# Kernel tuning notes

Measured on AMD Instinct MI355X. Metric: run time of the kernel, lower is better.

## Reference

```python
import jax, jax.numpy as jnp
import numpy as np
from jax import lax

B = 32768
IMG = 28
K = 3
OUT_HW = IMG - K + 1  # 26
FLAT = OUT_HW * OUT_HW  # 676
HID = 300
NCLS = 10


def setup_inputs() -> dict:
    key = jax.random.key(0)
    ks = jax.random.split(key, 8)
    x = jax.random.normal(ks[0], (B, IMG * IMG), dtype=jnp.float32)
    conv_w = jax.random.normal(ks[1], (K, K), dtype=jnp.float32) * 0.1
    # Linear params stored as (in, out) so forward is h @ W + b
    W1 = jax.random.normal(ks[2], (FLAT, HID), dtype=jnp.float32) * 0.04
    b1 = jnp.zeros((HID,), dtype=jnp.float32)
    W2 = jax.random.normal(ks[3], (HID, HID), dtype=jnp.float32) * 0.06
    b2 = jnp.zeros((HID,), dtype=jnp.float32)
    W3 = jax.random.normal(ks[4], (HID, NCLS), dtype=jnp.float32) * 0.06
    b3 = jnp.zeros((NCLS,), dtype=jnp.float32)
    return {"x": x, "conv_w": conv_w, "W1": W1, "b1": b1,
            "W2": W2, "b2": b2, "W3": W3, "b3": b3}


def reference(x, conv_w, W1, b1, W2, b2, W3, b3):
    b = x.shape[0]
    img = x.reshape(b, 1, IMG, IMG)  # NCHW
    # Valid cross-correlation with 3x3 kernel -> [B,1,26,26]
    y = lax.conv_general_dilated(
        img, conv_w[None, None, :, :], window_strides=(1, 1), padding="VALID",
        dimension_numbers=("NCHW", "OIHW", "NCHW"))
    h = y.reshape(b, FLAT)
    h = jax.nn.relu(h @ W1 + b1)
    h = jax.nn.relu(h @ W2 + b2)
    return h @ W3 + b3
```

## Files before the change

### kernel.cpp

```cpp
#include <hip/hip_runtime.h>


typedef __bf16 bf16_t;
typedef __bf16 bf16x8 __attribute__((ext_vector_type(8)));
typedef float  f32x4  __attribute__((ext_vector_type(4)));

#define MFMA16(a, b, c) __builtin_amdgcn_mfma_f32_16x16x32_bf16((a), (b), (c), 0, 0, 0)

#define W1F_ELEMS (25 * 20 * 64 * 8)
#define W2F_ELEMS (10 * 20 * 64 * 8)
#define W3F_ELEMS (10 * 1 * 64 * 8)

__global__ void prep_weights(const float* __restrict__ conv_w,
                             const float* __restrict__ W1,
                             const float* __restrict__ W2,
                             const float* __restrict__ W3,
                             bf16_t* __restrict__ W1f,
                             bf16_t* __restrict__ W2f,
                             bf16_t* __restrict__ W3f) {
    int idx = blockIdx.x * 256 + threadIdx.x;
    if (idx < 800 * 320) {
        int k = idx / 320;
        int n = idx - k * 320;
        float v = 0.0f;
        if (k < 784 && n < 300) {
            int py = k / 28;
            int px = k - py * 28;
#pragma unroll
            for (int ky = 0; ky < 3; ++ky) {
                int oy = py - ky;
                if (oy < 0 || oy > 25) continue;
#pragma unroll
                for (int kx = 0; kx < 3; ++kx) {
                    int ox = px - kx;
                    if (ox < 0 || ox > 25) continue;
                    v += conv_w[ky * 3 + kx] * W1[(oy * 26 + ox) * 300 + n];
                }
            }
        }
        int kc = k >> 5, quad = (k >> 3) & 3, j = k & 7;
        int nt = n >> 4, nin = n & 15;
        W1f[(((kc * 20 + nt) * 64 + quad * 16 + nin) << 3) + j] = (bf16_t)v;
    } else if (idx < 800 * 320 + 320 * 320) {
        int i2 = idx - 800 * 320;
        int k = i2 / 320;
        int n = i2 - k * 320;
        float v = (k < 300 && n < 300) ? W2[k * 300 + n] : 0.0f;
        int kc = k >> 5, quad = (k >> 3) & 3, j = k & 7;
        int nt = n >> 4, nin = n & 15;
        W2f[(((kc * 20 + nt) * 64 + quad * 16 + nin) << 3) + j] = (bf16_t)v;
    } else if (idx < 800 * 320 + 320 * 320 + 320 * 16) {
        int i3 = idx - (800 * 320 + 320 * 320);
        int k = i3 / 16;
        int n = i3 - k * 16;
        float v = (k < 300 && n < 10) ? W3[k * 10 + n] : 0.0f;
        int kc = k >> 5, quad = (k >> 3) & 3, j = k & 7;
        W3f[(((kc * 64) + quad * 16 + n) << 3) + j] = (bf16_t)v;
    }
}

__global__ __launch_bounds__(256, 2) void fused_mlp(
    const float* __restrict__ x, const float* __restrict__ b1,
    const float* __restrict__ b2, const float* __restrict__ b3,
    const bf16x8* __restrict__ W1f, const bf16x8* __restrict__ W2f,
    const bf16x8* __restrict__ W3f, float* __restrict__ out) {
    __shared__ bf16x8 bufA[4 * 64];
    __shared__ bf16x8 hbuf[10 * 4 * 64];

    const int tid = threadIdx.x;
    const int w = tid >> 6;
    const int l = tid & 63;
    const int r0 = blockIdx.x * 64;

    const int sr = tid >> 2;
    const int sg = tid & 3;
    const int s_mt = sr >> 4;
    const int s_lane = sg * 16 + (sr & 15);
    const float* xrow = x + (size_t)(r0 + sr) * 784;

    f32x4 acc[4][5];
#pragma unroll
    for (int mt = 0; mt < 4; ++mt)
#pragma unroll
        for (int nt = 0; nt < 5; ++nt) acc[mt][nt] = (f32x4){0.f, 0.f, 0.f, 0.f};

    float4 u0, u1;
    {
        int k0 = sg * 8;
        const float4* p = (const float4*)(xrow + k0);
        u0 = p[0];
        u1 = p[1];
    }
    for (int kc = 0; kc < 25; ++kc) {
        bf16x8 af;
        af[0] = (bf16_t)u0.x; af[1] = (bf16_t)u0.y;
        af[2] = (bf16_t)u0.z; af[3] = (bf16_t)u0.w;
        af[4] = (bf16_t)u1.x; af[5] = (bf16_t)u1.y;
        af[6] = (bf16_t)u1.z; af[7] = (bf16_t)u1.w;
        bufA[s_mt * 64 + s_lane] = af;
        __syncthreads();
        if (kc + 1 < 25) {
            int k0 = (kc + 1) * 32 + sg * 8;
            if (k0 < 784) {
                const float4* p = (const float4*)(xrow + k0);
                u0 = p[0];
                u1 = p[1];
            } else {
                u0 = make_float4(0.f, 0.f, 0.f, 0.f);
                u1 = make_float4(0.f, 0.f, 0.f, 0.f);
            }
        }
        bf16x8 a0 = bufA[0 * 64 + l];
        bf16x8 a1 = bufA[1 * 64 + l];
        bf16x8 a2 = bufA[2 * 64 + l];
        bf16x8 a3 = bufA[3 * 64 + l];
        const bf16x8* wb = W1f + (size_t)(kc * 20 + w * 5) * 64 + l;
#pragma unroll
        for (int nt = 0; nt < 5; ++nt) {
            bf16x8 b = wb[nt * 64];
            acc[0][nt] = MFMA16(a0, b, acc[0][nt]);
            acc[1][nt] = MFMA16(a1, b, acc[1][nt]);
            acc[2][nt] = MFMA16(a2, b, acc[2][nt]);
            acc[3][nt] = MFMA16(a3, b, acc[3][nt]);
        }
        __syncthreads();
    }

    {
        bf16_t* hb = (bf16_t*)hbuf;
#pragma unroll
        for (int nt = 0; nt < 5; ++nt) {
            int n = (w * 5 + nt) * 16 + (l & 15);
            float bias = (n < 300) ? b1[n] : 0.0f;
            int kc2 = n >> 5, quad = (n >> 3) & 3, j = n & 7;
#pragma unroll
            for (int mt = 0; mt < 4; ++mt) {
#pragma unroll
                for (int r = 0; r < 4; ++r) {
                    int row15 = (l >> 4) * 4 + r;
                    float v = acc[mt][nt][r] + bias;
                    v = v > 0.f ? v : 0.f;
                    hb[(((kc2 * 4 + mt) * 64 + quad * 16 + row15) << 3) + j] = (bf16_t)v;
                }
            }
        }
    }
    __syncthreads();

#pragma unroll
    for (int mt = 0; mt < 4; ++mt)
#pragma unroll
        for (int nt = 0; nt < 5; ++nt) acc[mt][nt] = (f32x4){0.f, 0.f, 0.f, 0.f};
    for (int kc = 0; kc < 10; ++kc) {
        bf16x8 a0 = hbuf[(kc * 4 + 0) * 64 + l];
        bf16x8 a1 = hbuf[(kc * 4 + 1) * 64 + l];
        bf16x8 a2 = hbuf[(kc * 4 + 2) * 64 + l];
        bf16x8 a3 = hbuf[(kc * 4 + 3) * 64 + l];
        const bf16x8* wb = W2f + (size_t)(kc * 20 + w * 5) * 64 + l;
#pragma unroll
        for (int nt = 0; nt < 5; ++nt) {
            bf16x8 b = wb[nt * 64];
            acc[0][nt] = MFMA16(a0, b, acc[0][nt]);
            acc[1][nt] = MFMA16(a1, b, acc[1][nt]);
            acc[2][nt] = MFMA16(a2, b, acc[2][nt]);
            acc[3][nt] = MFMA16(a3, b, acc[3][nt]);
        }
    }
    __syncthreads();

    {
        bf16_t* hb = (bf16_t*)hbuf;
#pragma unroll
        for (int nt = 0; nt < 5; ++nt) {
            int n = (w * 5 + nt) * 16 + (l & 15);
            float bias = (n < 300) ? b2[n] : 0.0f;
            int kc2 = n >> 5, quad = (n >> 3) & 3, j = n & 7;
#pragma unroll
            for (int mt = 0; mt < 4; ++mt) {
#pragma unroll
                for (int r = 0; r < 4; ++r) {
                    int row15 = (l >> 4) * 4 + r;
                    float v = acc[mt][nt][r] + bias;
                    v = v > 0.f ? v : 0.f;
                    hb[(((kc2 * 4 + mt) * 64 + quad * 16 + row15) << 3) + j] = (bf16_t)v;
                }
            }
        }
    }
    __syncthreads();

    f32x4 acc3 = (f32x4){0.f, 0.f, 0.f, 0.f};
    for (int kc = 0; kc < 10; ++kc) {
        bf16x8 a = hbuf[(kc * 4 + w) * 64 + l];
        bf16x8 b = W3f[kc * 64 + l];
        acc3 = MFMA16(a, b, acc3);
    }
    int n = l & 15;
    if (n < 10) {
        float bias = b3[n];
#pragma unroll
        for (int r = 0; r < 4; ++r) {
            int row = r0 + w * 16 + (l >> 4) * 4 + r;
            out[row * 10 + n] = acc3[r] + bias;
        }
    }
}

extern "C" void kernel_launch(void* const* d_in, const int* in_sizes, int n_in,
                              void* d_out, int out_size, void* d_ws, size_t ws_size,
                              hipStream_t stream) {
    const float* x      = (const float*)d_in[0];
    const float* conv_w = (const float*)d_in[1];
    const float* W1     = (const float*)d_in[2];
    const float* b1     = (const float*)d_in[3];
    const float* W2     = (const float*)d_in[4];
    const float* b2     = (const float*)d_in[5];
    const float* W3     = (const float*)d_in[6];
    const float* b3     = (const float*)d_in[7];
    float* out = (float*)d_out;

    char* ws = (char*)d_ws;
    bf16_t* W1f = (bf16_t*)(ws);
    bf16_t* W2f = (bf16_t*)(ws + (size_t)W1F_ELEMS * 2);
    bf16_t* W3f = (bf16_t*)(ws + (size_t)(W1F_ELEMS + W2F_ELEMS) * 2);
    if (ws_size < (size_t)(W1F_ELEMS + W2F_ELEMS + W3F_ELEMS) * 2) return;

    int prep_total = 800 * 320 + 320 * 320 + 320 * 16;
    prep_weights<<<(prep_total + 255) / 256, 256, 0, stream>>>(
        conv_w, W1, W2, W3, W1f, W2f, W3f);

    fused_mlp<<<32768 / 64, 256, 0, stream>>>(
        x, b1, b2, b3, (const bf16x8*)W1f, (const bf16x8*)W2f,
        (const bf16x8*)W3f, out);
}
```

Measured before the change: 198.0 us.

## Stage weights into LDS via async global_load_lds and split waves across M/N

Doubles the block to 512 threads with 8 waves, each owning half the 64 rows and a quarter of the output columns. Layer-1 weight tiles are double-buffered into LDS with global_load_lds, so they are fetched once per block rather than once per wave. Activation fragments are now loaded straight from global memory into MFMA layout, with no LDS staging. Layer-2 and layer-3 weights are also staged through a shared LDS arena that aliases the hidden buffer; the cost is more barriers in layer 2 and a different occupancy profile.

After: 202.2 us. 2.1% more time.

```diff
diff --git a/kernel.cpp b/kernel.cpp
--- a/kernel.cpp
+++ b/kernel.cpp
@@ -59,149 +59,176 @@
     }
 }
 
-__global__ __launch_bounds__(256, 2) void fused_mlp(
+__device__ __forceinline__ void stage16(const bf16x8* g, bf16x8* l) {
+    __builtin_amdgcn_global_load_lds(
+        (const __attribute__((address_space(1))) void*)g,
+        (__attribute__((address_space(3))) void*)l, 16, 0, 0);
+}
+
+__global__ __launch_bounds__(512, 4) void fused_mlp(
     const float* __restrict__ x, const float* __restrict__ b1,
     const float* __restrict__ b2, const float* __restrict__ b3,
     const bf16x8* __restrict__ W1f, const bf16x8* __restrict__ W2f,
     const bf16x8* __restrict__ W3f, float* __restrict__ out) {
-    __shared__ bf16x8 bufA[4 * 64];
-    __shared__ bf16x8 hbuf[10 * 4 * 64];
+    __shared__ bf16x8 arena[3840];
+    bf16x8* bufB1 = arena;
+    bf16x8* hbuf  = arena;
+    bf16x8* bufB2 = arena + 2560;
 
     const int tid = threadIdx.x;
-    const int w = tid >> 6;
-    const int l = tid & 63;
-    const int r0 = blockIdx.x * 64;
-
-    const int sr = tid >> 2;
-    const int sg = tid & 3;
-    const int s_mt = sr >> 4;
-    const int s_lane = sg * 16 + (sr & 15);
-    const float* xrow = x + (size_t)(r0 + sr) * 784;
-
-    f32x4 acc[4][5];
-#pragma unroll
-    for (int mt = 0; mt < 4; ++mt)
-#pragma unroll
-        for (int nt = 0; nt < 5; ++nt) acc[mt][nt] = (f32x4){0.f, 0.f, 0.f, 0.f};
-
-    float4 u0, u1;
+    const int w   = tid >> 6;
+    const int l   = tid & 63;
+    const int mh  = w & 1;
+    const int nq  = w >> 1;
+    const int q   = l >> 4;
+    const int l15 = l & 15;
+    const int r0  = blockIdx.x * 64;
+
+    const float* rowA = x + (size_t)(r0 + mh * 32 + l15) * 784;
+    const float* rowB = rowA + 16 * 784;
+
+    float bias1[5], bias2[5];
+#pragma unroll
+    for (int nt = 0; nt < 5; ++nt) {
+        int n = (nq * 5 + nt) * 16 + l15;
+        bias1[nt] = (n < 300) ? b1[n] : 0.0f;
+        bias2[nt] = (n < 300) ? b2[n] : 0.0f;
+    }
+    float bias3 = (w < 4 && l15 < 10) ? b3[l15] : 0.0f;
+
+    for (int t = w; t < 20; t += 8) stage16(W1f + (t * 64 + l), bufB1 + t * 64);
+    for (int t = w; t < 20; t += 8) stage16(W2f + (t * 64 + l), bufB2 + t * 64);
+
+    float4 ua0, ua1, ub0, ub1;
     {
-        int k0 = sg * 8;
-        const float4* p = (const float4*)(xrow + k0);
-        u0 = p[0];
-        u1 = p[1];
-    }
+        const float4* pa = (const float4*)(rowA + q * 8);
+        const float4* pb = (const float4*)(rowB + q * 8);
+        ua0 = pa[0]; ua1 = pa[1]; ub0 = pb[0]; ub1 = pb[1];
+    }
+
+    f32x4 acc[2][5];
+#pragma unroll
+    for (int m = 0; m < 2; ++m)
+#pragma unroll
+        for (int nt = 0; nt < 5; ++nt) acc[m][nt] = (f32x4){0.f, 0.f, 0.f, 0.f};
+
     for (int kc = 0; kc < 25; ++kc) {
-        bf16x8 af;
-        af[0] = (bf16_t)u0.x; af[1] = (bf16_t)u0.y;
-        af[2] = (bf16_t)u0.z; af[3] = (bf16_t)u0.w;
-        af[4] = (bf16_t)u1.x; af[5] = (bf16_t)u1.y;
-        af[6] = (bf16_t)u1.z; af[7] = (bf16_t)u1.w;
-        bufA[s_mt * 64 + s_lane] = af;
         __syncthreads();
+
         if (kc + 1 < 25) {
-            int k0 = (kc + 1) * 32 + sg * 8;
+            int s1 = (kc + 1) & 1;
+            for (int t = w; t < 20; t += 8)
+                stage16(W1f + (((kc + 1) * 20 + t) * 64 + l),
+                        bufB1 + s1 * 1280 + t * 64);
+        }
+
+        bf16x8 afA, afB;
+        afA[0] = (bf16_t)ua0.x; afA[1] = (bf16_t)ua0.y;
+        afA[2] = (bf16_t)ua0.z; afA[3] = (bf16_t)ua0.w;
+        afA[4] = (bf16_t)ua1.x; afA[5] = (bf16_t)ua1.y;
+        afA[6] = (bf16_t)ua1.z; afA[7] = (bf16_t)ua1.w;
+        afB[0] = (bf16_t)ub0.x; afB[1] = (bf16_t)ub0.y;
+        afB[2] = (bf16_t)ub0.z; afB[3] = (bf16_t)ub0.w;
+        afB[4] = (bf16_t)ub1.x; afB[5] = (bf16_t)ub1.y;
+        afB[6] = (bf16_t)ub1.z; afB[7] = (bf16_t)ub1.w;
+
+        if (kc + 1 < 25) {
+            int k0 = (kc + 1) * 32 + q * 8;
             if (k0 < 784) {
-                const float4* p = (const float4*)(xrow + k0);
-                u0 = p[0];
-                u1 = p[1];
+                const float4* pa = (const float4*)(rowA + k0);
+                const float4* pb = (const float4*)(rowB + k0);
+                ua0 = pa[0]; ua1 = pa[1]; ub0 = pb[0]; ub1 = pb[1];
             } else {
-                u0 = make_float4(0.f, 0.f, 0.f, 0.f);
-                u1 = make_float4(0.f, 0.f, 0.f, 0.f);
-            }
-        }
-        bf16x8 a0 = bufA[0 * 64 + l];
-        bf16x8 a1 = bufA[1 * 64 + l];
-        bf16x8 a2 = bufA[2 * 64 + l];
-        bf16x8 a3 = bufA[3 * 64 + l];
-        const bf16x8* wb = W1f + (size_t)(kc * 20 + w * 5) * 64 + l;
-#pragma unroll
-        for (int nt = 0; nt < 5; ++nt) {
-            bf16x8 b = wb[nt * 64];
+                ua0 = ua1 = ub0 = ub1 = make_float4(0.f, 0.f, 0.f, 0.f);
+            }
+        }
+
+        const bf16x8* bb = bufB1 + (kc & 1) * 1280 + (nq * 5) * 64 + l;
+#pragma unroll
+        for (int nt = 0; nt < 5; ++nt) {
+            bf16x8 b = bb[nt * 64];
+            acc[0][nt] = MFMA16(afA, b, acc[0][nt]);
+            acc[1][nt] = MFMA16(afB, b, acc[1][nt]);
+        }
+    }
+    __syncthreads();
+
+    {
+        bf16_t* hb = (bf16_t*)hbuf;
+#pragma unroll
+        for (int nt = 0; nt < 5; ++nt) {
+            int n = (nq * 5 + nt) * 16 + l15;
+            int kc2 = n >> 5, quad = (n >> 3) & 3, j = n & 7;
+#pragma unroll
+            for (int mt2 = 0; mt2 < 2; ++mt2) {
+                int mt = mh * 2 + mt2;
+#pragma unroll
+                for (int r = 0; r < 4; ++r) {
+                    float v = acc[mt2][nt][r] + bias1[nt];
+                    v = v > 0.f ? v : 0.f;
+                    hb[(((kc2 * 4 + mt) * 64 + quad * 16 + q * 4 + r) << 3) + j] =
+                        (bf16_t)v;
+                }
+            }
+        }
+    }
+    __syncthreads();
+
+#pragma unroll
+    for (int m = 0; m < 2; ++m)
+#pragma unroll
+        for (int nt = 0; nt < 5; ++nt) acc[m][nt] = (f32x4){0.f, 0.f, 0.f, 0.f};
+    for (int kc = 0; kc < 10; ++kc) {
+        bf16x8 a0 = hbuf[(kc * 4 + mh * 2 + 0) * 64 + l];
+        bf16x8 a1 = hbuf[(kc * 4 + mh * 2 + 1) * 64 + l];
+        const bf16x8* bb = bufB2 + (nq * 5) * 64 + l;
+#pragma unroll
+        for (int nt = 0; nt < 5; ++nt) {
+            bf16x8 b = bb[nt * 64];
             acc[0][nt] = MFMA16(a0, b, acc[0][nt]);
             acc[1][nt] = MFMA16(a1, b, acc[1][nt]);
-            acc[2][nt] = MFMA16(a2, b, acc[2][nt]);
-            acc[3][nt] = MFMA16(a3, b, acc[3][nt]);
-        }
-        __syncthreads();
-    }
+        }
+        if (kc + 1 < 10) {
+            __syncthreads();
+            for (int t = w; t < 20; t += 8)
+                stage16(W2f + (((kc + 1) * 20 + t) * 64 + l), bufB2 + t * 64);
+            __syncthreads();
+        }
+    }
+    __syncthreads();
 
     {
         bf16_t* hb = (bf16_t*)hbuf;
 #pragma unroll
         for (int nt = 0; nt < 5; ++nt) {
-            int n = (w * 5 + nt) * 16 + (l & 15);
-            float bias = (n < 300) ? b1[n] : 0.0f;
+            int n = (nq * 5 + nt) * 16 + l15;
             int kc2 = n >> 5, quad = (n >> 3) & 3, j = n & 7;
 #pragma unroll
-            for (int mt = 0; mt < 4; ++mt) {
+            for (int mt2 = 0; mt2 < 2; ++mt2) {
+                int mt = mh * 2 + mt2;
 #pragma unroll
                 for (int r = 0; r < 4; ++r) {
-                    int row15 = (l >> 4) * 4 + r;
-                    float v = acc[mt][nt][r] + bias;
+                    float v = acc[mt2][nt][r] + bias2[nt];
                     v = v > 0.f ? v : 0.f;
-                    hb[(((kc2 * 4 + mt) * 64 + quad * 16 + row15) << 3) + j] = (bf16_t)v;
+                    hb[(((kc2 * 4 + mt) * 64 + quad * 16 + q * 4 + r) << 3) + j] =
+                        (bf16_t)v;
                 }
             }
         }
     }
     __syncthreads();
 
-#pragma unroll
-    for (int mt = 0; mt < 4; ++mt)
-#pragma unroll
-        for (int nt = 0; nt < 5; ++nt) acc[mt][nt] = (f32x4){0.f, 0.f, 0.f, 0.f};
-    for (int kc = 0; kc < 10; ++kc) {
-        bf16x8 a0 = hbuf[(kc * 4 + 0) * 64 + l];
-        bf16x8 a1 = hbuf[(kc * 4 + 1) * 64 + l];
-        bf16x8 a2 = hbuf[(kc * 4 + 2) * 64 + l];
-        bf16x8 a3 = hbuf[(kc * 4 + 3) * 64 + l];
-        const bf16x8* wb = W2f + (size_t)(kc * 20 + w * 5) * 64 + l;
-#pragma unroll
-        for (int nt = 0; nt < 5; ++nt) {
-            bf16x8 b = wb[nt * 64];
-            acc[0][nt] = MFMA16(a0, b, acc[0][nt]);
-            acc[1][nt] = MFMA16(a1, b, acc[1][nt]);
-            acc[2][nt] = MFMA16(a2, b, acc[2][nt]);
-            acc[3][nt] = MFMA16(a3, b, acc[3][nt]);
-        }
-    }
-    __syncthreads();
-
-    {
-        bf16_t* hb = (bf16_t*)hbuf;
-#pragma unroll
-        for (int nt = 0; nt < 5; ++nt) {
-            int n = (w * 5 + nt) * 16 + (l & 15);
-            float bias = (n < 300) ? b2[n] : 0.0f;
-            int kc2 = n >> 5, quad = (n >> 3) & 3, j = n & 7;
-#pragma unroll
-            for (int mt = 0; mt < 4; ++mt) {
-#pragma unroll
-                for (int r = 0; r < 4; ++r) {
-                    int row15 = (l >> 4) * 4 + r;
-                    float v = acc[mt][nt][r] + bias;
-                    v = v > 0.f ? v : 0.f;
-                    hb[(((kc2 * 4 + mt) * 64 + quad * 16 + row15) << 3) + j] = (bf16_t)v;
-                }
-            }
-        }
-    }
-    __syncthreads();
-
-    f32x4 acc3 = (f32x4){0.f, 0.f, 0.f, 0.f};
-    for (int kc = 0; kc < 10; ++kc) {
-        bf16x8 a = hbuf[(kc * 4 + w) * 64 + l];
-        bf16x8 b = W3f[kc * 64 + l];
-        acc3 = MFMA16(a, b, acc3);
-    }
-    int n = l & 15;
-    if (n < 10) {
-        float bias = b3[n];
-#pragma unroll
-        for (int r = 0; r < 4; ++r) {
-            int row = r0 + w * 16 + (l >> 4) * 4 + r;
-            out[row * 10 + n] = acc3[r] + bias;
+    for (int t = w; t < 10; t += 8) stage16(W3f + (t * 64 + l), bufB2 + t * 64);
+    __syncthreads();
+
+    if (w < 4) {
+        f32x4 acc3 = (f32x4){0.f, 0.f, 0.f, 0.f};
+        for (int kc = 0; kc < 10; ++kc)
+            acc3 = MFMA16(hbuf[(kc * 4 + w) * 64 + l], bufB2[kc * 64 + l], acc3);
+        if (l15 < 10) {
+#pragma unroll
+            for (int r = 0; r < 4; ++r)
+                out[(size_t)(r0 + w * 16 + q * 4 + r) * 10 + l15] = acc3[r] + bias3;
         }
     }
 }
@@ -229,7 +256,7 @@
     prep_weights<<<(prep_total + 255) / 256, 256, 0, stream>>>(
         conv_w, W1, W2, W3, W1f, W2f, W3f);
 
-    fused_mlp<<<32768 / 64, 256, 0, stream>>>(
+    fused_mlp<<<32768 / 64, 512, 0, stream>>>(
         x, b1, b2, b3, (const bf16x8*)W1f, (const bf16x8*)W2f,
         (const bf16x8*)W3f, out);
 }
```
